# Optimization experiments

Measured on AMD Instinct MI355X. Metric: run time of the kernel, lower is better.

The kernel has to match this reference:

```python
import jax, jax.numpy as jnp
import numpy as np

DIM_HEAD = 64
REL_POS_DIM_HEAD = 32
SCALE = DIM_HEAD ** (-0.5)
REL_POS_SCALE = REL_POS_DIM_HEAD ** (-0.5)


def setup_inputs() -> dict:
    key = jax.random.key(0)
    k1, k2, k3, k4, k5 = jax.random.split(key, 5)
    B, H, S = 2, 16, 2048
    keys = jax.random.normal(k1, (B, H, S, DIM_HEAD), dtype=jnp.float32)
    queries = jax.random.normal(k2, (B, H, S, DIM_HEAD), dtype=jnp.float32)
    pos_key = jax.random.normal(k3, (B, H, S, REL_POS_DIM_HEAD), dtype=jnp.float32)
    pos_query = jax.random.normal(k4, (B, H, S, REL_POS_DIM_HEAD), dtype=jnp.float32)
    mask = jax.random.randint(k5, (B, S), 0, 2).astype(jnp.bool_)
    return {"keys": keys, "queries": queries, "pos_key": pos_key,
            "pos_query": pos_query, "mask": mask}


def reference(keys, queries, pos_key, pos_query, mask) -> jnp.ndarray:
    # clamp inputs to [-5, 5] as in the original module
    k = jnp.clip(keys, -5.0, 5.0)
    q = jnp.clip(queries, -5.0, 5.0)
    # content scores: [B, H, Q, K]
    dots = jnp.einsum("bhqd,bhkd->bhqk", q, k) * SCALE
    # relative-position scores
    pk = jnp.clip(pos_key, -5.0, 5.0)
    pq = jnp.clip(pos_query, -5.0, 5.0)
    dots = dots + jnp.einsum("bhqd,bhkd->bhqk", pq, pk) * REL_POS_SCALE
    # mask: True keys are not attended to; broadcast (B, K) -> (B, 1, 1, K)
    dots = jnp.where(mask[:, None, None, :], -jnp.inf, dots)
    return jax.nn.softmax(dots, axis=-1)
```

## Files before the change

### kernel.cpp

```cpp
#include <hip/hip_runtime.h>
#include <cstdint>
#include <cstddef>

#define SEQ 2048
#define TILES 16
#define FRAG_SHORTS 12288
#define FRAG_BYTES  24576

typedef __attribute__((ext_vector_type(8))) short bf16x8;
typedef __attribute__((ext_vector_type(4))) float f32x4;
typedef __attribute__((ext_vector_type(4))) short short4v;

__device__ __forceinline__ short f2bf(float f) {
    union { float f; unsigned u; } a; a.f = f;
    unsigned r = a.u + 0x7fffu + ((a.u >> 16) & 1u);
    return (short)(r >> 16);
}
__device__ __forceinline__ float clip5(float v) { return fminf(fmaxf(v, -5.0f), 5.0f); }
__device__ __forceinline__ float bflo2f(unsigned u) { union { unsigned u; float f; } a; a.u = u << 16; return a.f; }
__device__ __forceinline__ float bfhi2f(unsigned u) { union { unsigned u; float f; } a; a.u = u & 0xffff0000u; return a.f; }

__global__ __launch_bounds__(256)
void prep_kernel(const float* __restrict__ Kp, const float* __restrict__ PKp,
                 short* __restrict__ wsK)
{
    int id = blockIdx.x * 256 + threadIdx.x;
    int q = id % 24;
    int row = id / 24;
    int bh = row >> 11;
    int col = row & 2047;
    int tile = col >> 7;
    int st = (col >> 4) & 7;
    int l15 = col & 15;
    float4 v;
    int f, dd;
    if (q < 16) {
        v = reinterpret_cast<const float4*>(Kp)[(size_t)row * 16 + q];
        f = q >> 3;
        dd = (q & 7) * 4;
    } else {
        v = reinterpret_cast<const float4*>(PKp)[(size_t)row * 8 + (q - 16)];
        f = 2;
        dd = (q - 16) * 4;
    }
    int ll = l15 | ((dd >> 3) << 4);
    int j = dd & 7;
    short4v s4;
    s4[0] = f2bf(clip5(v.x)); s4[1] = f2bf(clip5(v.y));
    s4[2] = f2bf(clip5(v.z)); s4[3] = f2bf(clip5(v.w));
    *reinterpret_cast<short4v*>(wsK + ((size_t)bh * TILES + tile) * FRAG_SHORTS
                                + (((st * 3 + f) * 64 + ll) << 3) + j) = s4;
}

#define CSTEP(kb0, kb1, kb2, T, STI, ST) do {                                        \
    f32x4 madd4 = *reinterpret_cast<const f32x4*>(&lds_madd[(T) * 128 + (ST) * 16 + l4 * 4]); \
    f32x4 acc = {0.f, 0.f, 0.f, 0.f};                                                \
    acc = __builtin_amdgcn_mfma_f32_16x16x32_bf16(kb0, qa[0], acc, 0, 0, 0);         \
    acc = __builtin_amdgcn_mfma_f32_16x16x32_bf16(kb1, qa[1], acc, 0, 0, 0);         \
    acc = __builtin_amdgcn_mfma_f32_16x16x32_bf16(kb2, qa[2], acc, 0, 0, 0);         \
    float e0 = exp2f(acc[0] - SHIFT + madd4[0]);                                     \
    float e1 = exp2f(acc[1] - SHIFT + madd4[1]);                                     \
    float e2 = exp2f(acc[2] - SHIFT + madd4[2]);                                     \
    float e3 = exp2f(acc[3] - SHIFT + madd4[3]);                                     \
    ssum += (e0 + e1) + (e2 + e3);                                                   \
    unsigned u0, u1;                                                                 \
    asm("v_cvt_pk_bf16_f32 %0, %1, %2" : "=v"(u0) : "v"(e0), "v"(e1));               \
    asm("v_cvt_pk_bf16_f32 %0, %1, %2" : "=v"(u1) : "v"(e2), "v"(e3));               \
    pk[(T) * 4 + (STI) * 2]     = u0;                                                \
    pk[(T) * 4 + (STI) * 2 + 1] = u1;                                                \
} while (0)

template<bool USEWS>
__global__ __launch_bounds__(512, 4)
void attn_map_kernel(const float* __restrict__ Kp, const float* __restrict__ Qp,
                     const float* __restrict__ PKp, const float* __restrict__ PQp,
                     const int* __restrict__ maskp, const short* __restrict__ wsK,
                     float* __restrict__ out)
{
    __shared__ short lds_k[2][FRAG_SHORTS];
    __shared__ float lds_madd[SEQ];
    __shared__ float sred[8][16];

    const int p = blockIdx.x;
    const int x = p & 7;
    const int slot = p >> 3;
    const int bh = x + 8 * (slot >> 6);
    const int qb = slot & 63;

    const int tid = threadIdx.x;
    const int lane = tid & 63;
    const int w = tid >> 6;
    const int l15 = lane & 15;
    const int l4 = lane >> 4;
    const int rg = w & 1;
    const int cs = w >> 1;

    const int qrow = qb * 32 + rg * 16 + l15;

    const float* Qb  = Qp  + (size_t)bh * (SEQ * 64);
    const float* PQb = PQp + (size_t)bh * (SEQ * 32);
    const int*   mb  = maskp + (size_t)(bh >> 4) * SEQ;
    float* orow = out + (size_t)bh * SEQ * SEQ + (size_t)qrow * SEQ;

    const float QS  = 0.125f * 1.4426950408889634f;
    const float PQS = 0.17677669529663687f * 1.4426950408889634f;
    const float SHIFT = 28.853900817779268f;

    bf16x8 qa[3];
    #pragma unroll
    for (int f = 0; f < 2; ++f) {
        const float* src = Qb + (size_t)qrow * 64 + f * 32 + l4 * 8;
        bf16x8 v;
        #pragma unroll
        for (int j = 0; j < 8; ++j) v[j] = f2bf(clip5(src[j]) * QS);
        qa[f] = v;
    }
    {
        const float* src = PQb + (size_t)qrow * 32 + l4 * 8;
        bf16x8 v;
        #pragma unroll
        for (int j = 0; j < 8; ++j) v[j] = f2bf(clip5(src[j]) * PQS);
        qa[2] = v;
    }

    #pragma unroll
    for (int i = 0; i < SEQ / 512; ++i) {
        int idx = i * 512 + tid;
        lds_madd[idx] = mb[idx] ? -1e30f : 0.0f;
    }

    const short* kf = USEWS ? (wsK + (size_t)bh * (TILES * FRAG_SHORTS)) : nullptr;

    unsigned pk[64];
    float ssum = 0.0f;

    if constexpr (USEWS) {
        #pragma unroll
        for (int c = 0; c < 3; ++c) {
            int off = w * 3072 + c * 1024;
            __builtin_amdgcn_global_load_lds(
                (const __attribute__((address_space(1))) void*)((const char*)kf + off + lane * 16),
                (__attribute__((address_space(3))) void*)((char*)&lds_k[0][0] + off),
                16, 0, 0);
        }
    } else {
        #pragma unroll
        for (int i = 0; i < 6; ++i) {
            int e = i * 512 + tid;
            int col = e / 24, dq = e - col * 24, d0 = dq * 4;
            float4 v; int f, dd;
            if (d0 < 64) {
                v = *reinterpret_cast<const float4*>(Kp + (size_t)bh * (SEQ * 64) + (size_t)col * 64 + d0);
                f = d0 >> 5; dd = d0 & 31;
            } else {
                v = *reinterpret_cast<const float4*>(PKp + (size_t)bh * (SEQ * 32) + (size_t)col * 32 + (d0 - 64));
                f = 2; dd = d0 - 64;
            }
            int ll = (col & 15) | ((dd >> 3) << 4);
            int st2 = col >> 4, j = dd & 7;
            short4v s4;
            s4[0] = f2bf(clip5(v.x)); s4[1] = f2bf(clip5(v.y));
            s4[2] = f2bf(clip5(v.z)); s4[3] = f2bf(clip5(v.w));
            *reinterpret_cast<short4v*>(&lds_k[0][(((st2 * 3 + f) * 64 + ll) << 3) + j]) = s4;
        }
    }
    __syncthreads();

    #pragma unroll
    for (int t = 0; t < TILES; ++t) {
        if (t + 1 < TILES) {
            if constexpr (USEWS) {
                const char* ksrc = (const char*)kf + (size_t)(t + 1) * FRAG_BYTES;
                #pragma unroll
                for (int c = 0; c < 3; ++c) {
                    int off = w * 3072 + c * 1024;
                    __builtin_amdgcn_global_load_lds(
                        (const __attribute__((address_space(1))) void*)(ksrc + off + lane * 16),
                        (__attribute__((address_space(3))) void*)((char*)&lds_k[(t + 1) & 1][0] + off),
                        16, 0, 0);
                }
            } else {
                const int tile0 = (t + 1) * 128;
                #pragma unroll
                for (int i = 0; i < 6; ++i) {
                    int e = i * 512 + tid;
                    int col = e / 24, dq = e - col * 24, d0 = dq * 4;
                    int colg = tile0 + col;
                    float4 v; int f, dd;
                    if (d0 < 64) {
                        v = *reinterpret_cast<const float4*>(Kp + (size_t)bh * (SEQ * 64) + (size_t)colg * 64 + d0);
                        f = d0 >> 5; dd = d0 & 31;
                    } else {
                        v = *reinterpret_cast<const float4*>(PKp + (size_t)bh * (SEQ * 32) + (size_t)colg * 32 + (d0 - 64));
                        f = 2; dd = d0 - 64;
                    }
                    int ll = (col & 15) | ((dd >> 3) << 4);
                    int st2 = col >> 4, j = dd & 7;
                    short4v s4;
                    s4[0] = f2bf(clip5(v.x)); s4[1] = f2bf(clip5(v.y));
                    s4[2] = f2bf(clip5(v.z)); s4[3] = f2bf(clip5(v.w));
                    *reinterpret_cast<short4v*>(&lds_k[(t + 1) & 1][(((st2 * 3 + f) * 64 + ll) << 3) + j]) = s4;
                }
            }
        }
        const short* lk = &lds_k[t & 1][0];
        #pragma unroll
        for (int sti = 0; sti < 2; ++sti) {
            const int st = cs * 2 + sti;
            bf16x8 kb0 = *reinterpret_cast<const bf16x8*>(lk + ((st * 3 + 0) * 64 + lane) * 8);
            bf16x8 kb1 = *reinterpret_cast<const bf16x8*>(lk + ((st * 3 + 1) * 64 + lane) * 8);
            bf16x8 kb2 = *reinterpret_cast<const bf16x8*>(lk + ((st * 3 + 2) * 64 + lane) * 8);
            CSTEP(kb0, kb1, kb2, t, sti, st);
        }
        __syncthreads();
    }

    float s = ssum;
    s += __shfl_xor(s, 16);
    s += __shfl_xor(s, 32);
    if (lane < 16) sred[w][l15] = s;
    __syncthreads();
    const float rs = sred[rg][l15] + sred[2 + rg][l15] + sred[4 + rg][l15] + sred[6 + rg][l15];
    const float inv = 1.0f / rs;

    #pragma unroll
    for (int t = 0; t < TILES; ++t) {
        #pragma unroll
        for (int sti = 0; sti < 2; ++sti) {
            unsigned u0 = pk[t * 4 + sti * 2];
            unsigned u1 = pk[t * 4 + sti * 2 + 1];
            f32x4 pv = { bflo2f(u0) * inv, bfhi2f(u0) * inv,
                         bflo2f(u1) * inv, bfhi2f(u1) * inv };
            *reinterpret_cast<f32x4*>(orow + t * 128 + (cs * 2 + sti) * 16 + l4 * 4) = pv;
        }
    }
}

extern "C" void kernel_launch(void* const* d_in, const int* in_sizes, int n_in,
                              void* d_out, int out_size, void* d_ws, size_t ws_size,
                              hipStream_t stream) {
    const float* keys      = (const float*)d_in[0];
    const float* queries   = (const float*)d_in[1];
    const float* pos_key   = (const float*)d_in[2];
    const float* pos_query = (const float*)d_in[3];
    const int*   mask      = (const int*)d_in[4];
    float* outp = (float*)d_out;

    const size_t need = (size_t)32 * TILES * FRAG_SHORTS * sizeof(short);
    if (ws_size >= need) {
        short* wsK = (short*)d_ws;
        prep_kernel<<<dim3(6144), dim3(256), 0, stream>>>(keys, pos_key, wsK);
        attn_map_kernel<true><<<dim3(2048), dim3(512), 0, stream>>>(
            keys, queries, pos_key, pos_query, mask, wsK, outp);
    } else {
        attn_map_kernel<false><<<dim3(2048), dim3(512), 0, stream>>>(
            keys, queries, pos_key, pos_query, mask, nullptr, outp);
    }
}
```

Measured before the change: 184.0 us.

## Use 16 query rows per block with one key subtile per wave

Each block now handles 16 query rows instead of 32. Each of the 8 waves takes one 16-key subtile per 128-key tile, and the grid doubles to 4096 blocks. This halves the per-thread packed-probability registers, which should ease register pressure and raise occupancy. The cost is that each K tile staged in LDS is reused by half as many queries, so K-tile global/LDS traffic doubles, and the row-sum reduction now spans all 8 waves.

```diff
diff --git a/kernel.cpp b/kernel.cpp
--- a/kernel.cpp
+++ b/kernel.cpp
@@ -52,24 +52,6 @@
                                 + (((st * 3 + f) * 64 + ll) << 3) + j) = s4;
 }
 
-#define CSTEP(kb0, kb1, kb2, T, STI, ST) do {                                        \
-    f32x4 madd4 = *reinterpret_cast<const f32x4*>(&lds_madd[(T) * 128 + (ST) * 16 + l4 * 4]); \
-    f32x4 acc = {0.f, 0.f, 0.f, 0.f};                                                \
-    acc = __builtin_amdgcn_mfma_f32_16x16x32_bf16(kb0, qa[0], acc, 0, 0, 0);         \
-    acc = __builtin_amdgcn_mfma_f32_16x16x32_bf16(kb1, qa[1], acc, 0, 0, 0);         \
-    acc = __builtin_amdgcn_mfma_f32_16x16x32_bf16(kb2, qa[2], acc, 0, 0, 0);         \
-    float e0 = exp2f(acc[0] - SHIFT + madd4[0]);                                     \
-    float e1 = exp2f(acc[1] - SHIFT + madd4[1]);                                     \
-    float e2 = exp2f(acc[2] - SHIFT + madd4[2]);                                     \
-    float e3 = exp2f(acc[3] - SHIFT + madd4[3]);                                     \
-    ssum += (e0 + e1) + (e2 + e3);                                                   \
-    unsigned u0, u1;                                                                 \
-    asm("v_cvt_pk_bf16_f32 %0, %1, %2" : "=v"(u0) : "v"(e0), "v"(e1));               \
-    asm("v_cvt_pk_bf16_f32 %0, %1, %2" : "=v"(u1) : "v"(e2), "v"(e3));               \
-    pk[(T) * 4 + (STI) * 2]     = u0;                                                \
-    pk[(T) * 4 + (STI) * 2 + 1] = u1;                                                \
-} while (0)
-
 template<bool USEWS>
 __global__ __launch_bounds__(512, 4)
 void attn_map_kernel(const float* __restrict__ Kp, const float* __restrict__ Qp,
@@ -84,18 +66,16 @@
     const int p = blockIdx.x;
     const int x = p & 7;
     const int slot = p >> 3;
-    const int bh = x + 8 * (slot >> 6);
-    const int qb = slot & 63;
+    const int bh = x + 8 * (slot >> 7);
+    const int qb = slot & 127;
 
     const int tid = threadIdx.x;
     const int lane = tid & 63;
     const int w = tid >> 6;
     const int l15 = lane & 15;
     const int l4 = lane >> 4;
-    const int rg = w & 1;
-    const int cs = w >> 1;
-
-    const int qrow = qb * 32 + rg * 16 + l15;
+
+    const int qrow = qb * 16 + l15;
 
     const float* Qb  = Qp  + (size_t)bh * (SEQ * 64);
     const float* PQb = PQp + (size_t)bh * (SEQ * 32);
@@ -131,7 +111,7 @@
 
     const short* kf = USEWS ? (wsK + (size_t)bh * (TILES * FRAG_SHORTS)) : nullptr;
 
-    unsigned pk[64];
+    unsigned pk[32];
     float ssum = 0.0f;
 
     if constexpr (USEWS) {
@@ -204,13 +184,25 @@
             }
         }
         const short* lk = &lds_k[t & 1][0];
-        #pragma unroll
-        for (int sti = 0; sti < 2; ++sti) {
-            const int st = cs * 2 + sti;
-            bf16x8 kb0 = *reinterpret_cast<const bf16x8*>(lk + ((st * 3 + 0) * 64 + lane) * 8);
-            bf16x8 kb1 = *reinterpret_cast<const bf16x8*>(lk + ((st * 3 + 1) * 64 + lane) * 8);
-            bf16x8 kb2 = *reinterpret_cast<const bf16x8*>(lk + ((st * 3 + 2) * 64 + lane) * 8);
-            CSTEP(kb0, kb1, kb2, t, sti, st);
+        {
+            bf16x8 kb0 = *reinterpret_cast<const bf16x8*>(lk + ((w * 3 + 0) * 64 + lane) * 8);
+            bf16x8 kb1 = *reinterpret_cast<const bf16x8*>(lk + ((w * 3 + 1) * 64 + lane) * 8);
+            bf16x8 kb2 = *reinterpret_cast<const bf16x8*>(lk + ((w * 3 + 2) * 64 + lane) * 8);
+            f32x4 madd4 = *reinterpret_cast<const f32x4*>(&lds_madd[t * 128 + w * 16 + l4 * 4]);
+            f32x4 acc = {0.f, 0.f, 0.f, 0.f};
+            acc = __builtin_amdgcn_mfma_f32_16x16x32_bf16(kb0, qa[0], acc, 0, 0, 0);
+            acc = __builtin_amdgcn_mfma_f32_16x16x32_bf16(kb1, qa[1], acc, 0, 0, 0);
+            acc = __builtin_amdgcn_mfma_f32_16x16x32_bf16(kb2, qa[2], acc, 0, 0, 0);
+            float e0 = exp2f(acc[0] - SHIFT + madd4[0]);
+            float e1 = exp2f(acc[1] - SHIFT + madd4[1]);
+            float e2 = exp2f(acc[2] - SHIFT + madd4[2]);
+            float e3 = exp2f(acc[3] - SHIFT + madd4[3]);
+            ssum += (e0 + e1) + (e2 + e3);
+            unsigned u0, u1;
+            asm("v_cvt_pk_bf16_f32 %0, %1, %2" : "=v"(u0) : "v"(e0), "v"(e1));
+            asm("v_cvt_pk_bf16_f32 %0, %1, %2" : "=v"(u1) : "v"(e2), "v"(e3));
+            pk[t * 2]     = u0;
+            pk[t * 2 + 1] = u1;
         }
         __syncthreads();
     }
@@ -220,19 +212,17 @@
     s += __shfl_xor(s, 32);
     if (lane < 16) sred[w][l15] = s;
     __syncthreads();
-    const float rs = sred[rg][l15] + sred[2 + rg][l15] + sred[4 + rg][l15] + sred[6 + rg][l15];
+    const float rs = ((sred[0][l15] + sred[1][l15]) + (sred[2][l15] + sred[3][l15]))
+                   + ((sred[4][l15] + sred[5][l15]) + (sred[6][l15] + sred[7][l15]));
     const float inv = 1.0f / rs;
 
     #pragma unroll
     for (int t = 0; t < TILES; ++t) {
-        #pragma unroll
-        for (int sti = 0; sti < 2; ++sti) {
-            unsigned u0 = pk[t * 4 + sti * 2];
-            unsigned u1 = pk[t * 4 + sti * 2 + 1];
-            f32x4 pv = { bflo2f(u0) * inv, bfhi2f(u0) * inv,
-                         bflo2f(u1) * inv, bfhi2f(u1) * inv };
-            *reinterpret_cast<f32x4*>(orow + t * 128 + (cs * 2 + sti) * 16 + l4 * 4) = pv;
-        }
+        unsigned u0 = pk[t * 2];
+        unsigned u1 = pk[t * 2 + 1];
+        f32x4 pv = { bflo2f(u0) * inv, bfhi2f(u0) * inv,
+                     bflo2f(u1) * inv, bfhi2f(u1) * inv };
+        *reinterpret_cast<f32x4*>(orow + t * 128 + w * 16 + l4 * 4) = pv;
     }
 }
 
@@ -250,10 +240,10 @@
     if (ws_size >= need) {
         short* wsK = (short*)d_ws;
         prep_kernel<<<dim3(6144), dim3(256), 0, stream>>>(keys, pos_key, wsK);
-        attn_map_kernel<true><<<dim3(2048), dim3(512), 0, stream>>>(
+        attn_map_kernel<true><<<dim3(4096), dim3(512), 0, stream>>>(
             keys, queries, pos_key, pos_query, mask, wsK, outp);
     } else {
-        attn_map_kernel<false><<<dim3(2048), dim3(512), 0, stream>>>(
+        attn_map_kernel<false><<<dim3(4096), dim3(512), 0, stream>>>(
             keys, queries, pos_key, pos_query, mask, nullptr, outp);
     }
 }
```

After: 210.8 us. 1.15x slower.
